# Optimization experiments

Hardware: AMD Instinct MI355X
Metric: run time of the kernel (lower is better)

## Reference

```python
import jax, jax.numpy as jnp
import numpy as np

N_E, E_DIM = 2048, 256
B, H, W = 32, 32, 32


def setup_inputs() -> dict:
    key = jax.random.key(0)
    k1, k2 = jax.random.split(key)
    z = jax.random.normal(k1, (B, E_DIM, H, W), dtype=jnp.float32)
    embedding = jax.random.normal(k2, (N_E, E_DIM), dtype=jnp.float32)
    return {"z": z, "embedding": embedding}


def reference(z, embedding):
    # z: [B, C, H, W] with C == e_dim; embedding: [n_e, e_dim]
    n_e, e_dim = embedding.shape
    b, c, h, w = z.shape
    z_nhwc = jnp.transpose(z, (0, 2, 3, 1))            # [B,H,W,C]
    z_flat = z_nhwc.reshape(-1, e_dim)                 # [L, D]
    # squared euclidean distance: ||z||^2 + ||e||^2 - 2 z.e^T
    d = (
        jnp.sum(z_flat * z_flat, axis=1, keepdims=True)
        + jnp.sum(embedding * embedding, axis=1)
        - 2.0 * jnp.einsum("ld,nd->ln", z_flat, embedding)
    )                                                  # [L, n_e]
    idx = jnp.argmin(d, axis=1)                        # [L]
    z_q = jnp.take(embedding, idx, axis=0).reshape(b, h, w, e_dim)
    # embed_ema=True -> commitment-only loss (codebook updated by EMA, not grads)
    loss = jnp.mean((jax.lax.stop_gradient(z_q) - z_nhwc) ** 2)
    # straight-through estimator
    z_q_st = z_nhwc + jax.lax.stop_gradient(z_q - z_nhwc)
    quantize = jnp.transpose(z_q_st, (0, 3, 1, 2))     # [B,C,H,W]
    # number of distinct codebook entries used (jit-safe via scatter-set)
    used = jnp.sum(jnp.zeros((n_e,), z.dtype).at[idx].set(1.0))
    index = idx.reshape(b, h, w)
    return quantize, loss, index, used
```

## Files before the change

kernel.cpp:

```cpp
#include <hip/hip_runtime.h>
#include <cfloat>

#define Dm 256
#define HW 1024
#define NE 2048
#define L_TOT 32768
#define QOFF 8388608
#define TAU 0.02f

typedef __attribute__((ext_vector_type(8))) short bf16x8;
typedef __attribute__((ext_vector_type(4))) float f32x4;
typedef const __attribute__((address_space(1))) unsigned int* as1_u32p;
typedef __attribute__((address_space(3))) unsigned int* as3_u32p;

#define GLL(gp, lp) __builtin_amdgcn_global_load_lds((as1_u32p)(gp), (as3_u32p)(lp), 16, 0, 0)

__device__ __forceinline__ unsigned short f2bf(float x) {
    unsigned u = __float_as_uint(x);
    unsigned r = (u + 0x7fffu + ((u >> 16) & 1u)) >> 16;
    return (unsigned short)r;
}
__device__ __forceinline__ float bf2f(unsigned short h) {
    return __uint_as_float(((unsigned)h) << 16);
}

__global__ void k_enorm(const float* __restrict__ emb, float* __restrict__ enorm) {
    int w = threadIdx.x >> 6, lane = threadIdx.x & 63;
    int n = blockIdx.x * 4 + w;
    const float4 v = *reinterpret_cast<const float4*>(emb + (size_t)n * Dm + lane * 4);
    double s = (double)v.x * v.x + (double)v.y * v.y + (double)v.z * v.z + (double)v.w * v.w;
    #pragma unroll
    for (int off = 32; off; off >>= 1) s += __shfl_xor(s, off);
    if (lane == 0) enorm[n] = (float)s;
}

__global__ __launch_bounds__(256) void k_split(
    const float* __restrict__ z, const float* __restrict__ emb,
    unsigned short* __restrict__ z_hi, unsigned short* __restrict__ z_lo,
    unsigned short* __restrict__ e_hi, unsigned short* __restrict__ e_lo,
    float* __restrict__ enorm, float* __restrict__ zn_part,
    float* __restrict__ used, int* __restrict__ flag_cnt)
{
    __shared__ unsigned short zh[32][260];
    __shared__ unsigned short zl[32][260];
    __shared__ double zsum[4];
    const int t = threadIdx.x;
    const int w = t >> 6, lane = t & 63;

    if (blockIdx.x >= 16 && blockIdx.x < 24) used[(blockIdx.x - 16) * 256 + t] = 0.f;
    if (blockIdx.x == 24 && t == 0) *flag_cnt = 0;

    if (w < 2) {
        int n = blockIdx.x * 2 + w;
        const float4 v = *reinterpret_cast<const float4*>(emb + (size_t)n * Dm + lane * 4);
        float vv[4] = { v.x, v.y, v.z, v.w };
        double s = (double)v.x * v.x + (double)v.y * v.y + (double)v.z * v.z + (double)v.w * v.w;
        #pragma unroll
        for (int off = 32; off; off >>= 1) s += __shfl_xor(s, off);
        if (lane == 0) enorm[n] = (float)s;
        ushort4 h4, l4;
        unsigned short* hp = (unsigned short*)&h4;
        unsigned short* lp = (unsigned short*)&l4;
        #pragma unroll
        for (int j = 0; j < 4; ++j) {
            unsigned short h = f2bf(vv[j]);
            hp[j] = h;
            lp[j] = f2bf(vv[j] - bf2f(h));
        }
        *reinterpret_cast<ushort4*>(e_hi + (size_t)n * Dm + lane * 4) = h4;
        *reinterpret_cast<ushort4*>(e_lo + (size_t)n * Dm + lane * 4) = l4;
    }

    const int b  = blockIdx.x >> 5;
    const int p0 = (blockIdx.x & 31) * 32;
    const int pp = t & 31, cb = t >> 5;
    const float* zb = z + (size_t)b * (Dm * HW) + p0 + pp;
    float zs = 0.f;
    for (int ci = 0; ci < 32; ++ci) {
        int c = ci * 8 + cb;
        float x = zb[(size_t)c * HW];
        zs = fmaf(x, x, zs);
        unsigned short h = f2bf(x);
        zh[pp][c] = h;
        zl[pp][c] = f2bf(x - bf2f(h));
    }
    double d = zs;
    #pragma unroll
    for (int off = 32; off; off >>= 1) d += __shfl_xor(d, off);
    if ((t & 63) == 0) zsum[w] = d;
    __syncthreads();
    if (t == 0) zn_part[blockIdx.x] = (float)(zsum[0] + zsum[1] + zsum[2] + zsum[3]);
    const int l0 = b * 1024 + p0;
    #pragma unroll
    for (int r = 0; r < 8; ++r) {
        int id = r * 256 + t;
        int row = id >> 6, ch = id & 63;
        *reinterpret_cast<ushort4*>(z_hi + (size_t)(l0 + row) * Dm + ch * 4) =
            *reinterpret_cast<ushort4*>(&zh[row][ch * 4]);
        *reinterpret_cast<ushort4*>(z_lo + (size_t)(l0 + row) * Dm + ch * 4) =
            *reinterpret_cast<ushort4*>(&zl[row][ch * 4]);
    }
}

__global__ __launch_bounds__(512, 4) void k_score2(
    const unsigned short* __restrict__ z_hi, const unsigned short* __restrict__ z_lo,
    const unsigned short* __restrict__ e_hi, const unsigned short* __restrict__ e_lo,
    const float* __restrict__ enorm,
    float* __restrict__ pd1, float* __restrict__ pd2, int* __restrict__ pi1)
{
    __shared__ unsigned short lds[2][2][128 * 64];

    const int t    = threadIdx.x;
    const int lane = t & 63, w = t >> 6;
    const int wm = w >> 2, wn = w & 3;
    const int c15 = lane & 15, g4 = lane >> 4;

    const int bx = blockIdx.x;
    const int wg = (bx & 7) * 64 + (bx >> 3);
    const int mi = wg >> 1, ni = wg & 1;
    const int l0 = mi * 128;
    const int nbase = ni * 1024;

    auto stage = [&](int buf, const unsigned short* As, const unsigned short* Bs,
                     int nB0, int k0) {
        #pragma unroll
        for (int r = 0; r < 2; ++r) {
            int id  = r * 512 + t;
            int row = id >> 3, ch = id & 7;
            int chg = ch ^ (row & 7);
            GLL(As + (size_t)(l0 + row) * Dm + k0 + chg * 8, &lds[buf][0][id * 8]);
            GLL(Bs + (size_t)(nB0 + row) * Dm + k0 + chg * 8, &lds[buf][1][id * 8]);
        }
    };

    float d1[4][4], d2[4][4]; int i1[4][4];
    #pragma unroll
    for (int m = 0; m < 4; ++m)
        #pragma unroll
        for (int r = 0; r < 4; ++r) { d1[m][r] = 3.4e38f; d2[m][r] = 3.4e38f; i1[m][r] = 0; }

    stage(0, z_hi, e_hi, nbase, 0);
    __syncthreads();

    int cur = 0, it = 0;
    for (int nt = 0; nt < 8; ++nt) {
        f32x4 acc[4][2];
        #pragma unroll
        for (int m = 0; m < 4; ++m)
            #pragma unroll
            for (int n = 0; n < 2; ++n) acc[m][n] = (f32x4){0.f, 0.f, 0.f, 0.f};

        for (int kt = 0; kt < 12; ++kt, ++it) {
            if (it + 1 < 96) {
                int nit = it + 1;
                int nnt = nit / 12;
                int nkt = nit - nnt * 12;
                int nterm = nkt >> 2, nkc = nkt & 3;
                const unsigned short* As = (nterm == 1) ? z_lo : z_hi;
                const unsigned short* Bs = (nterm == 2) ? e_lo : e_hi;
                stage(cur ^ 1, As, Bs, nbase + nnt * 128, nkc * 64);
            }
            const unsigned short* Ab = &lds[cur][0][0];
            const unsigned short* Bb = &lds[cur][1][0];
            #pragma unroll
            for (int ks = 0; ks < 2; ++ks) {
                bf16x8 af[4], bfr[2];
                #pragma unroll
                for (int m = 0; m < 4; ++m) {
                    int row = wm * 64 + m * 16 + c15;
                    int cc  = ks * 4 + g4;
                    af[m] = *reinterpret_cast<const bf16x8*>(
                        &Ab[row * 64 + ((cc ^ (row & 7)) << 3)]);
                }
                #pragma unroll
                for (int n = 0; n < 2; ++n) {
                    int row = wn * 32 + n * 16 + c15;
                    int cc  = ks * 4 + g4;
                    bfr[n] = *reinterpret_cast<const bf16x8*>(
                        &Bb[row * 64 + ((cc ^ (row & 7)) << 3)]);
                }
                __builtin_amdgcn_s_setprio(1);
                #pragma unroll
                for (int m = 0; m < 4; ++m)
                    #pragma unroll
                    for (int n = 0; n < 2; ++n)
                        acc[m][n] = __builtin_amdgcn_mfma_f32_16x16x32_bf16(
                            af[m], bfr[n], acc[m][n], 0, 0, 0);
                __builtin_amdgcn_s_setprio(0);
            }
            __syncthreads();
            cur ^= 1;
        }
        int n0 = nbase + nt * 128;
        #pragma unroll
        for (int n = 0; n < 2; ++n) {
            int ng = n0 + wn * 32 + n * 16 + c15;
            float en = enorm[ng];
            #pragma unroll
            for (int m = 0; m < 4; ++m)
                #pragma unroll
                for (int r = 0; r < 4; ++r) {
                    float s = fmaf(-2.f, acc[m][n][r], en);
                    if (s < d1[m][r]) { d2[m][r] = d1[m][r]; d1[m][r] = s; i1[m][r] = ng; }
                    else if (s < d2[m][r]) d2[m][r] = s;
                }
        }
    }

    #pragma unroll
    for (int off = 1; off <= 8; off <<= 1) {
        #pragma unroll
        for (int m = 0; m < 4; ++m)
            #pragma unroll
            for (int r = 0; r < 4; ++r) {
                float od1 = __shfl_xor(d1[m][r], off);
                int   oi1 = __shfl_xor(i1[m][r], off);
                float od2 = __shfl_xor(d2[m][r], off);
                float nd2 = fminf(fminf(d2[m][r], od2), fmaxf(d1[m][r], od1));
                if (od1 < d1[m][r] || (od1 == d1[m][r] && oi1 < i1[m][r])) {
                    d1[m][r] = od1; i1[m][r] = oi1;
                }
                d2[m][r] = nd2;
            }
    }

    float* rs1 = (float*)&lds[0][0][0];
    float* rs2 = rs1 + 3 * 128;
    int*   ri  = (int*)(rs2 + 3 * 128);
    if (wn > 0 && c15 == 0) {
        int s = wn - 1;
        #pragma unroll
        for (int m = 0; m < 4; ++m)
            #pragma unroll
            for (int r = 0; r < 4; ++r) {
                int q = wm * 64 + m * 16 + g4 * 4 + r;
                rs1[s * 128 + q] = d1[m][r];
                rs2[s * 128 + q] = d2[m][r];
                ri [s * 128 + q] = i1[m][r];
            }
    }
    __syncthreads();
    if (wn == 0 && c15 == 0) {
        #pragma unroll
        for (int m = 0; m < 4; ++m)
            #pragma unroll
            for (int r = 0; r < 4; ++r) {
                int q = wm * 64 + m * 16 + g4 * 4 + r;
                float bd1 = d1[m][r], bd2 = d2[m][r]; int bi1 = i1[m][r];
                #pragma unroll
                for (int s = 0; s < 3; ++s) {
                    float od1 = rs1[s * 128 + q], od2 = rs2[s * 128 + q];
                    int   oi1 = ri [s * 128 + q];
                    float nd2 = fminf(fminf(bd2, od2), fmaxf(bd1, od1));
                    if (od1 < bd1 || (od1 == bd1 && oi1 < bi1)) { bd1 = od1; bi1 = oi1; }
                    bd2 = nd2;
                }
                int gq = l0 + q;
                pd1[ni * L_TOT + gq] = bd1;
                pd2[ni * L_TOT + gq] = bd2;
                pi1[ni * L_TOT + gq] = bi1;
            }
    }
}

__global__ __launch_bounds__(256) void k_mg(
    const float* __restrict__ pd1, const float* __restrict__ pd2,
    const int* __restrict__ pi1, const float* __restrict__ emb,
    int* __restrict__ ws_idx, float* __restrict__ out_idxf,
    float* __restrict__ used, int* __restrict__ flag_cnt,
    int* __restrict__ flag_list, float* __restrict__ d1_part,
    float* __restrict__ outq)
{
    __shared__ int sidx[64];
    __shared__ float eldT[Dm][65];
    const int t = threadIdx.x;
    const int l0 = blockIdx.x * 64;
    const int b = l0 >> 10, p0 = l0 & 1023;

    if (t < 64) {
        int gq = l0 + t;
        float d1 = pd1[gq], d2 = pd2[gq]; int i1 = pi1[gq];
        float od1 = pd1[L_TOT + gq], od2 = pd2[L_TOT + gq];
        int   oi1 = pi1[L_TOT + gq];
        float nd2 = fminf(fminf(d2, od2), fmaxf(d1, od1));
        if (od1 < d1 || (od1 == d1 && oi1 < i1)) { d1 = od1; i1 = oi1; }
        d2 = nd2;
        ws_idx[gq] = i1;
        out_idxf[gq] = (float)i1;
        if (d2 - d1 < TAU) {
            int pos = atomicAdd(flag_cnt, 1);
            flag_list[pos] = gq;
        } else {
            used[i1] = 1.0f;
        }
        sidx[t] = i1;
        float s = d1;
        #pragma unroll
        for (int off = 32; off; off >>= 1) s += __shfl_xor(s, off);
        if (t == 0) d1_part[blockIdx.x] = s;
    }
    __syncthreads();

    int w = t >> 6, lane = t & 63;
    for (int r = 0; r < 16; ++r) {
        int q = r * 4 + w;
        const float4 v = *reinterpret_cast<const float4*>(emb + (size_t)sidx[q] * Dm + lane * 4);
        eldT[lane * 4 + 0][q] = v.x; eldT[lane * 4 + 1][q] = v.y;
        eldT[lane * 4 + 2][q] = v.z; eldT[lane * 4 + 3][q] = v.w;
    }
    __syncthreads();
    const size_t obase = (size_t)b * (Dm * HW) + p0 + lane;
    #pragma unroll 4
    for (int it = 0; it < 64; ++it) {
        int c = w * 64 + it;
        outq[obase + (size_t)c * HW] = eldT[c][lane];
    }
}

__global__ __launch_bounds__(256) void k_merge(
    const float* __restrict__ pd1, const float* __restrict__ pd2,
    const int* __restrict__ pi1, int* __restrict__ ws_idx,
    float* __restrict__ out_idxf, float* __restrict__ used,
    int* __restrict__ flag_cnt, int* __restrict__ flag_list,
    float* __restrict__ d1_part)
{
    __shared__ float sdl[256];
    int tt = threadIdx.x;
    int gq = blockIdx.x * 256 + tt;
    float d1 = pd1[gq], d2 = pd2[gq]; int i1 = pi1[gq];
    {
        float od1 = pd1[L_TOT + gq], od2 = pd2[L_TOT + gq];
        int   oi1 = pi1[L_TOT + gq];
        float nd2 = fminf(fminf(d2, od2), fmaxf(d1, od1));
        if (od1 < d1 || (od1 == d1 && oi1 < i1)) { d1 = od1; i1 = oi1; }
        d2 = nd2;
    }
    ws_idx[gq] = i1;
    out_idxf[gq] = (float)i1;
    if (d2 - d1 < TAU) {
        int pos = atomicAdd(flag_cnt, 1);
        flag_list[pos] = gq;
    } else {
        used[i1] = 1.0f;
    }
    sdl[tt] = d1;
    __syncthreads();
    for (int st = 128; st; st >>= 1) {
        if (tt < st) sdl[tt] += sdl[tt + st];
        __syncthreads();
    }
    if (tt == 0) d1_part[blockIdx.x] = sdl[0];
}

#define BM 64
#define BN 128
#define BK 64
__global__ __launch_bounds__(256, 2) void k_argmin_f32(
    const float* __restrict__ z, const float* __restrict__ emb,
    const float* __restrict__ enorm, int* __restrict__ ws_idx,
    float* __restrict__ out_idxf, float* __restrict__ used,
    int* __restrict__ flag_cnt, int* __restrict__ flag_list)
{
    __shared__ float zl[BK][BM];
    __shared__ float el[BK][BN + 4];
    __shared__ float rd1[4][64];
    __shared__ int   ri1[4][64];
    __shared__ float rd2[4][64];

    const int t  = threadIdx.x;
    const int tq = t & 15;
    const int tn = t >> 4;
    const int l0 = blockIdx.x * BM;
    const int b  = l0 >> 10, p0 = l0 & 1023;
    const float* zb = z + (size_t)b * (Dm * HW) + p0;

    float d1[4], d2[4]; int i1[4];
    #pragma unroll
    for (int i = 0; i < 4; ++i) { d1[i] = FLT_MAX; d2[i] = FLT_MAX; i1[i] = 0; }

    for (int nt = 0; nt < NE / BN; ++nt) {
        const int n0 = nt * BN;
        float acc[4][8];
        #pragma unroll
        for (int i = 0; i < 4; ++i)
            #pragma unroll
            for (int j = 0; j < 8; ++j) acc[i][j] = 0.f;

        for (int kc = 0; kc < Dm / BK; ++kc) {
            __syncthreads();
            #pragma unroll
            for (int r = 0; r < 4; ++r) {
                int f = r * 256 + t;
                int kk = f >> 4, q4 = (f & 15) << 2;
                float4 v = *reinterpret_cast<const float4*>(zb + (size_t)(kc * BK + kk) * HW + q4);
                *reinterpret_cast<float4*>(&zl[kk][q4]) = v;
            }
            #pragma unroll
            for (int r = 0; r < 8; ++r) {
                int f = r * 256 + t;
                int n = f >> 4, k4 = (f & 15) << 2;
                float4 v = *reinterpret_cast<const float4*>(emb + (size_t)(n0 + n) * Dm + kc * BK + k4);
                el[k4 + 0][n] = v.x; el[k4 + 1][n] = v.y;
                el[k4 + 2][n] = v.z; el[k4 + 3][n] = v.w;
            }
            __syncthreads();
            #pragma unroll 4
            for (int kk = 0; kk < BK; ++kk) {
                float4 zf = *reinterpret_cast<const float4*>(&zl[kk][tq << 2]);
                float4 e0 = *reinterpret_cast<const float4*>(&el[kk][tn << 3]);
                float4 e1 = *reinterpret_cast<const float4*>(&el[kk][(tn << 3) + 4]);
                float zr[4] = { zf.x, zf.y, zf.z, zf.w };
                float er[8] = { e0.x, e0.y, e0.z, e0.w, e1.x, e1.y, e1.z, e1.w };
                #pragma unroll
                for (int i = 0; i < 4; ++i)
                    #pragma unroll
                    for (int j = 0; j < 8; ++j)
                        acc[i][j] = fmaf(zr[i], er[j], acc[i][j]);
            }
        }
        #pragma unroll
        for (int j = 0; j < 8; ++j) {
            int ng = n0 + (tn << 3) + j;
            float en = enorm[ng];
            #pragma unroll
            for (int i = 0; i < 4; ++i) {
                float s = fmaf(-2.f, acc[i][j], en);
                if (s < d1[i]) { d2[i] = d1[i]; d1[i] = s; i1[i] = ng; }
                else if (s < d2[i]) d2[i] = s;
            }
        }
    }
    #pragma unroll
    for (int off = 16; off <= 32; off <<= 1) {
        #pragma unroll
        for (int i = 0; i < 4; ++i) {
            float od1 = __shfl_xor(d1[i], off);
            int   oi1 = __shfl_xor(i1[i], off);
            float od2 = __shfl_xor(d2[i], off);
            float nd2 = fminf(fminf(d2[i], od2), fmaxf(d1[i], od1));
            bool take = (od1 < d1[i]) || (od1 == d1[i] && oi1 < i1[i]);
            if (take) { d1[i] = od1; i1[i] = oi1; }
            d2[i] = nd2;
        }
    }
    int w = t >> 6;
    if ((t & 63) < 16) {
        #pragma unroll
        for (int i = 0; i < 4; ++i) {
            rd1[w][(tq << 2) + i] = d1[i];
            ri1[w][(tq << 2) + i] = i1[i];
            rd2[w][(tq << 2) + i] = d2[i];
        }
    }
    __syncthreads();
    if (t < 64) {
        float bd1 = rd1[0][t]; int bi1 = ri1[0][t]; float bd2 = rd2[0][t];
        #pragma unroll
        for (int ww = 1; ww < 4; ++ww) {
            float od1 = rd1[ww][t]; int oi1 = ri1[ww][t]; float od2 = rd2[ww][t];
            float nd2 = fminf(fminf(bd2, od2), fmaxf(bd1, od1));
            if (od1 < bd1 || (od1 == bd1 && oi1 < bi1)) { bd1 = od1; bi1 = oi1; }
            bd2 = nd2;
        }
        int l = l0 + t;
        ws_idx[l] = bi1;
        out_idxf[l] = (float)bi1;
        if (bd2 - bd1 < TAU) {
            int pos = atomicAdd(flag_cnt, 1);
            flag_list[pos] = l;
        } else {
            used[bi1] = 1.0f;
        }
    }
}

__global__ void k_refine(const float* __restrict__ z, const float* __restrict__ emb,
                         const int* __restrict__ flag_cnt, const int* __restrict__ flag_list,
                         int* __restrict__ ws_idx, float* __restrict__ out_idxf,
                         float* __restrict__ used, float* __restrict__ outq)
{
    __shared__ float zrow[Dm];
    __shared__ double sd[256];
    __shared__ int    si[256];
    int nf = *flag_cnt;
    for (int fi = blockIdx.x; fi < nf; fi += gridDim.x) {
        int l = flag_list[fi];
        int b = l >> 10, p = l & 1023;
        const float* zq = z + (size_t)b * (Dm * HW) + p;
        __syncthreads();
        for (int c = threadIdx.x; c < Dm; c += blockDim.x) zrow[c] = zq[(size_t)c * HW];
        __syncthreads();
        double bd = DBL_MAX; int bi = 0;
        for (int nb = 0; nb < NE / 256; ++nb) {
            int n = nb * 256 + threadIdx.x;
            const float* er = emb + (size_t)n * Dm;
            double dt0 = 0.0, dt1 = 0.0, dt2 = 0.0, dt3 = 0.0;
            double nm0 = 0.0, nm1 = 0.0, nm2 = 0.0, nm3 = 0.0;
            for (int c = 0; c < Dm; c += 4) {
                double e0 = er[c], e1 = er[c + 1], e2 = er[c + 2], e3 = er[c + 3];
                dt0 += e0 * (double)zrow[c];     nm0 += e0 * e0;
                dt1 += e1 * (double)zrow[c + 1]; nm1 += e1 * e1;
                dt2 += e2 * (double)zrow[c + 2]; nm2 += e2 * e2;
                dt3 += e3 * (double)zrow[c + 3]; nm3 += e3 * e3;
            }
            double s = (nm0 + nm1) + (nm2 + nm3) - 2.0 * ((dt0 + dt1) + (dt2 + dt3));
            if (s < bd) { bd = s; bi = n; }
        }
        sd[threadIdx.x] = bd; si[threadIdx.x] = bi;
        __syncthreads();
        for (int st = 128; st; st >>= 1) {
            if (threadIdx.x < (unsigned)st) {
                double od = sd[threadIdx.x + st]; int oi = si[threadIdx.x + st];
                if (od < sd[threadIdx.x] || (od == sd[threadIdx.x] && oi < si[threadIdx.x])) {
                    sd[threadIdx.x] = od; si[threadIdx.x] = oi;
                }
            }
            __syncthreads();
        }
        if (threadIdx.x == 0) {
            ws_idx[l] = si[0];
            out_idxf[l] = (float)si[0];
            used[si[0]] = 1.0f;
        }
        __syncthreads();
        int bi0 = si[0];
        int c = threadIdx.x;
        outq[(size_t)b * (Dm * HW) + (size_t)c * HW + p] = emb[(size_t)bi0 * Dm + c];
        __syncthreads();
    }
}

__global__ __launch_bounds__(256) void k_gather(
    const float* __restrict__ emb, const int* __restrict__ ws_idx,
    float* __restrict__ outq)
{
    __shared__ int sidx[64];
    __shared__ float eldT[Dm][65];
    const int t = threadIdx.x;
    const int l0 = blockIdx.x * 64;
    const int b = l0 >> 10, p0 = l0 & 1023;
    if (t < 64) sidx[t] = ws_idx[l0 + t];
    __syncthreads();
    int w = t >> 6, lane = t & 63;
    for (int r = 0; r < 16; ++r) {
        int q = r * 4 + w;
        const float4 v = *reinterpret_cast<const float4*>(emb + (size_t)sidx[q] * Dm + lane * 4);
        eldT[lane * 4 + 0][q] = v.x; eldT[lane * 4 + 1][q] = v.y;
        eldT[lane * 4 + 2][q] = v.z; eldT[lane * 4 + 3][q] = v.w;
    }
    __syncthreads();
    const size_t obase = (size_t)b * (Dm * HW) + p0 + lane;
    #pragma unroll 4
    for (int it = 0; it < 64; ++it) {
        int c = w * 64 + it;
        outq[obase + (size_t)c * HW] = eldT[c][lane];
    }
}

__global__ __launch_bounds__(256) void k_gather_loss(
    const float* __restrict__ z, const float* __restrict__ emb,
    const int* __restrict__ ws_idx, float* __restrict__ outq,
    float* __restrict__ partials)
{
    __shared__ int sidx[64];
    __shared__ float eldT[Dm][65];
    __shared__ float wsum[4];
    const int t = threadIdx.x;
    const int l0 = blockIdx.x * 64;
    const int b = l0 >> 10, p0 = l0 & 1023;
    if (t < 64) sidx[t] = ws_idx[l0 + t];
    __syncthreads();
    int w = t >> 6, lane = t & 63;
    for (int r = 0; r < 16; ++r) {
        int q = r * 4 + w;
        const float4 v = *reinterpret_cast<const float4*>(emb + (size_t)sidx[q] * Dm + lane * 4);
        eldT[lane * 4 + 0][q] = v.x; eldT[lane * 4 + 1][q] = v.y;
        eldT[lane * 4 + 2][q] = v.z; eldT[lane * 4 + 3][q] = v.w;
    }
    __syncthreads();
    float ls = 0.f;
    const size_t obase = (size_t)b * (Dm * HW) + p0 + lane;
    for (int it = 0; it < 64; ++it) {
        int c = w * 64 + it;
        size_t o = obase + (size_t)c * HW;
        float qv = eldT[c][lane];
        float zv = z[o];
        outq[o] = qv;
        float df = qv - zv;
        ls = fmaf(df, df, ls);
    }
    #pragma unroll
    for (int off = 32; off; off >>= 1) ls += __shfl_xor(ls, off);
    if (lane == 0) wsum[w] = ls;
    __syncthreads();
    if (t == 0) partials[blockIdx.x] = wsum[0] + wsum[1] + wsum[2] + wsum[3];
}

__global__ void k_final(const float* __restrict__ zn_part, const float* __restrict__ d1_part,
                        int nd1, const float* __restrict__ used,
                        float* __restrict__ out_loss, float* __restrict__ out_used)
{
    __shared__ double s1[256];
    __shared__ float  s2[256];
    int t = threadIdx.x;
    double a = 0.0;
    for (int i = t; i < 1024; i += 256) a += (double)zn_part[i];
    for (int i = t; i < nd1; i += 256) a += (double)d1_part[i];
    float u = 0.f;
    for (int i = t; i < NE; i += 256) u += used[i];
    s1[t] = a; s2[t] = u;
    __syncthreads();
    for (int st = 128; st; st >>= 1) {
        if (t < st) { s1[t] += s1[t + st]; s2[t] += s2[t + st]; }
        __syncthreads();
    }
    if (t == 0) { *out_loss = (float)(s1[0] / 8388608.0); *out_used = s2[0]; }
}

__global__ void k_final_fb(const float* __restrict__ partials, const float* __restrict__ used,
                           float* __restrict__ out_loss, float* __restrict__ out_used)
{
    __shared__ float s1[256], s2[256];
    int t = threadIdx.x;
    float a = partials[t] + partials[t + 256];
    float u = 0.f;
    for (int i = t; i < NE; i += 256) u += used[i];
    s1[t] = a; s2[t] = u;
    __syncthreads();
    for (int st = 128; st; st >>= 1) {
        if (t < st) { s1[t] += s1[t + st]; s2[t] += s2[t + st]; }
        __syncthreads();
    }
    if (t == 0) { *out_loss = s1[0] / 8388608.f; *out_used = s2[0]; }
}

extern "C" void kernel_launch(void* const* d_in, const int* in_sizes, int n_in,
                              void* d_out, int out_size, void* d_ws, size_t ws_size,
                              hipStream_t stream) {
    const float* z   = (const float*)d_in[0];
    const float* emb = (const float*)d_in[1];
    float* out      = (float*)d_out;
    float* outq     = out;
    float* out_loss = out + QOFF;
    float* out_idxf = out + QOFF + 1;
    float* out_used = out + QOFF + 1 + L_TOT;

    float* ws       = (float*)d_ws;
    float* enorm    = ws;
    float* used     = ws + 2048;
    float* zn_part  = ws + 4096;
    float* d1_part  = ws + 5120;
    int*   flag_cnt = (int*)(ws + 5632);
    int*   ws_idx   = (int*)(ws + 5888);
    int*   flag_list= (int*)(ws + 5888 + L_TOT);

    float* pd1w = ws + 71680;
    float* pd2w = ws + 137216;
    int*   pi1w = (int*)(ws + 202752);

    size_t bf_bytes = 2ull * (NE + L_TOT) * Dm * sizeof(unsigned short);
    size_t need_t1 = 268288ull * 4 + bf_bytes;
    size_t need_t2 = 71680ull * 4 + bf_bytes;

    if (ws_size >= need_t1) {
        unsigned short* e_hi = (unsigned short*)(ws + 268288);
        unsigned short* e_lo = e_hi + (size_t)NE * Dm;
        unsigned short* z_hi = e_lo + (size_t)NE * Dm;
        unsigned short* z_lo = z_hi + (size_t)L_TOT * Dm;
        k_split<<<1024, 256, 0, stream>>>(z, emb, z_hi, z_lo, e_hi, e_lo,
                                          enorm, zn_part, used, flag_cnt);
        k_score2<<<512, 512, 0, stream>>>(z_hi, z_lo, e_hi, e_lo, enorm, pd1w, pd2w, pi1w);
        k_mg<<<L_TOT / 64, 256, 0, stream>>>(pd1w, pd2w, pi1w, emb, ws_idx, out_idxf,
                                             used, flag_cnt, flag_list, d1_part, outq);
        k_refine<<<256, 256, 0, stream>>>(z, emb, flag_cnt, flag_list, ws_idx, out_idxf,
                                          used, outq);
        k_final<<<1, 256, 0, stream>>>(zn_part, d1_part, 512, used, out_loss, out_used);
    } else if (ws_size >= need_t2) {
        unsigned short* e_hi = (unsigned short*)(ws + 71680);
        unsigned short* e_lo = e_hi + (size_t)NE * Dm;
        unsigned short* z_hi = e_lo + (size_t)NE * Dm;
        unsigned short* z_lo = z_hi + (size_t)L_TOT * Dm;
        float* pd1 = outq;
        float* pd2 = outq + 2 * L_TOT;
        int*   pi1 = (int*)(outq + 4 * L_TOT);
        k_split<<<1024, 256, 0, stream>>>(z, emb, z_hi, z_lo, e_hi, e_lo,
                                          enorm, zn_part, used, flag_cnt);
        k_score2<<<512, 512, 0, stream>>>(z_hi, z_lo, e_hi, e_lo, enorm, pd1, pd2, pi1);
        k_merge<<<L_TOT / 256, 256, 0, stream>>>(pd1, pd2, pi1, ws_idx, out_idxf, used,
                                                 flag_cnt, flag_list, d1_part);
        k_refine<<<256, 256, 0, stream>>>(z, emb, flag_cnt, flag_list, ws_idx, out_idxf,
                                          used, outq);
        k_gather<<<L_TOT / 64, 256, 0, stream>>>(emb, ws_idx, outq);
        k_final<<<1, 256, 0, stream>>>(zn_part, d1_part, 128, used, out_loss, out_used);
    } else {
        hipMemsetAsync(used, 0, (size_t)3584 * 4, stream);
        k_enorm<<<NE / 4, 256, 0, stream>>>(emb, enorm);
        k_argmin_f32<<<L_TOT / BM, 256, 0, stream>>>(z, emb, enorm, ws_idx, out_idxf, used,
                                                     flag_cnt, flag_list);
        k_refine<<<256, 256, 0, stream>>>(z, emb, flag_cnt, flag_list, ws_idx, out_idxf,
                                          used, outq);
        k_gather_loss<<<L_TOT / 64, 256, 0, stream>>>(z, emb, ws_idx, outq, zn_part);
        k_final_fb<<<1, 256, 0, stream>>>(zn_part, used, out_loss, out_used);
    }
}
```

Measured before the change: 241.1 us.

## Restructure fp64 refine kernel to wave-per-code with shuffle reduction; tighten flag margin

The exact fp64 refinement kernel moves from one thread per codebook row, which made strided uncoalesced row reads, to one wavefront per codebook row. Each lane loads a float4 slice and the partial distances are combined with xor-shuffles, so loads are coalesced and the shared-memory tree reduction is replaced by a 4-way per-wave combine. The bf16 ambiguity threshold TAU is also halved, so fewer rows are flagged for refinement. That reduces refine work but risks missing true argmin ties when the bf16 error exceeds the new margin.

```diff
diff --git a/kernel.cpp b/kernel.cpp
--- a/kernel.cpp
+++ b/kernel.cpp
@@ -6,7 +6,7 @@
 #define NE 2048
 #define L_TOT 32768
 #define QOFF 8388608
-#define TAU 0.02f
+#define TAU 0.01f
 
 typedef __attribute__((ext_vector_type(8))) short bf16x8;
 typedef __attribute__((ext_vector_type(4))) float f32x4;
@@ -474,59 +474,54 @@
     }
 }
 
-__global__ void k_refine(const float* __restrict__ z, const float* __restrict__ emb,
-                         const int* __restrict__ flag_cnt, const int* __restrict__ flag_list,
-                         int* __restrict__ ws_idx, float* __restrict__ out_idxf,
-                         float* __restrict__ used, float* __restrict__ outq)
+__global__ __launch_bounds__(256) void k_refine(
+    const float* __restrict__ z, const float* __restrict__ emb,
+    const int* __restrict__ flag_cnt, const int* __restrict__ flag_list,
+    int* __restrict__ ws_idx, float* __restrict__ out_idxf,
+    float* __restrict__ used, float* __restrict__ outq)
 {
     __shared__ float zrow[Dm];
-    __shared__ double sd[256];
-    __shared__ int    si[256];
-    int nf = *flag_cnt;
+    __shared__ double wbd[4];
+    __shared__ int    wbi[4];
+    __shared__ int    bestn;
+    const int t = threadIdx.x, w = t >> 6, lane = t & 63;
+    const int nf = *flag_cnt;
     for (int fi = blockIdx.x; fi < nf; fi += gridDim.x) {
-        int l = flag_list[fi];
-        int b = l >> 10, p = l & 1023;
+        const int l = flag_list[fi];
+        const int b = l >> 10, p = l & 1023;
         const float* zq = z + (size_t)b * (Dm * HW) + p;
         __syncthreads();
-        for (int c = threadIdx.x; c < Dm; c += blockDim.x) zrow[c] = zq[(size_t)c * HW];
+        zrow[t] = zq[(size_t)t * HW];
         __syncthreads();
+        const double z0 = zrow[lane * 4 + 0], z1 = zrow[lane * 4 + 1];
+        const double z2 = zrow[lane * 4 + 2], z3 = zrow[lane * 4 + 3];
         double bd = DBL_MAX; int bi = 0;
-        for (int nb = 0; nb < NE / 256; ++nb) {
-            int n = nb * 256 + threadIdx.x;
-            const float* er = emb + (size_t)n * Dm;
-            double dt0 = 0.0, dt1 = 0.0, dt2 = 0.0, dt3 = 0.0;
-            double nm0 = 0.0, nm1 = 0.0, nm2 = 0.0, nm3 = 0.0;
-            for (int c = 0; c < Dm; c += 4) {
-                double e0 = er[c], e1 = er[c + 1], e2 = er[c + 2], e3 = er[c + 3];
-                dt0 += e0 * (double)zrow[c];     nm0 += e0 * e0;
-                dt1 += e1 * (double)zrow[c + 1]; nm1 += e1 * e1;
-                dt2 += e2 * (double)zrow[c + 2]; nm2 += e2 * e2;
-                dt3 += e3 * (double)zrow[c + 3]; nm3 += e3 * e3;
-            }
-            double s = (nm0 + nm1) + (nm2 + nm3) - 2.0 * ((dt0 + dt1) + (dt2 + dt3));
+        for (int n = w; n < NE; n += 4) {
+            const float4 e4 = *reinterpret_cast<const float4*>(emb + (size_t)n * Dm + lane * 4);
+            double e0 = e4.x, e1 = e4.y, e2 = e4.z, e3 = e4.w;
+            double s = e0 * (e0 - 2.0 * z0) + e1 * (e1 - 2.0 * z1)
+                     + e2 * (e2 - 2.0 * z2) + e3 * (e3 - 2.0 * z3);
+            #pragma unroll
+            for (int off = 1; off <= 32; off <<= 1) s += __shfl_xor(s, off);
             if (s < bd) { bd = s; bi = n; }
         }
-        sd[threadIdx.x] = bd; si[threadIdx.x] = bi;
+        if (lane == 0) { wbd[w] = bd; wbi[w] = bi; }
         __syncthreads();
-        for (int st = 128; st; st >>= 1) {
-            if (threadIdx.x < (unsigned)st) {
-                double od = sd[threadIdx.x + st]; int oi = si[threadIdx.x + st];
-                if (od < sd[threadIdx.x] || (od == sd[threadIdx.x] && oi < si[threadIdx.x])) {
-                    sd[threadIdx.x] = od; si[threadIdx.x] = oi;
+        if (t == 0) {
+            double b0 = wbd[0]; int i0 = wbi[0];
+            #pragma unroll
+            for (int ww = 1; ww < 4; ++ww) {
+                if (wbd[ww] < b0 || (wbd[ww] == b0 && wbi[ww] < i0)) {
+                    b0 = wbd[ww]; i0 = wbi[ww];
                 }
             }
-            __syncthreads();
-        }
-        if (threadIdx.x == 0) {
-            ws_idx[l] = si[0];
-            out_idxf[l] = (float)si[0];
-            used[si[0]] = 1.0f;
+            ws_idx[l] = i0;
+            out_idxf[l] = (float)i0;
+            used[i0] = 1.0f;
+            bestn = i0;
         }
         __syncthreads();
-        int bi0 = si[0];
-        int c = threadIdx.x;
-        outq[(size_t)b * (Dm * HW) + (size_t)c * HW + p] = emb[(size_t)bi0 * Dm + c];
-        __syncthreads();
+        outq[(size_t)b * (Dm * HW) + (size_t)t * HW + p] = emb[(size_t)bestn * Dm + t];
     }
 }
 
```

After: 412.0 us. 70.9% more time.
